# Kernel tuning notes

Hardware: AMD Instinct MI355X
Metric: run time of the kernel (lower is better)

The kernel has to match this reference:

```python
import jax, jax.numpy as jnp
import numpy as np
import math

B, S, CTX, D, H, DH = 2, 2048, 256, 1024, 16, 64
INNER = H * DH
DFF = 4 * D


def layernorm(x, eps=1e-5):
    m = jnp.mean(x, axis=-1, keepdims=True)
    v = jnp.var(x, axis=-1, keepdims=True)
    return (x - m) * jax.lax.rsqrt(v + eps)


def adaln(x, t, w, b):
    # AdaLayerNorm: linear(t) -> (scale, shift); NOTE: original never applies SiLU.
    emb = t @ w + b                       # [B,1,2D]
    scale, shift = jnp.split(emb, 2, axis=-1)
    return layernorm(x) * (1.0 + scale) + shift


def mha(xq, ctx, wq, wk, wv, wo, bo):
    b, sq, _ = xq.shape
    sk = ctx.shape[1]
    q = (xq @ wq).reshape(b, sq, H, DH).transpose(0, 2, 1, 3)   # bhqd
    k = (ctx @ wk).reshape(b, sk, H, DH).transpose(0, 2, 1, 3)  # bhkd
    v = (ctx @ wv).reshape(b, sk, H, DH).transpose(0, 2, 1, 3)
    scores = jnp.einsum('bhqd,bhkd->bhqk', q, k) / math.sqrt(DH)
    attn = jax.nn.softmax(scores, axis=-1)
    out = jnp.einsum('bhqk,bhkd->bhqd', attn, v)
    out = out.transpose(0, 2, 1, 3).reshape(b, sq, INNER)
    return out @ wo + bo


def glu_ff(x, w1, b1, w2, b2):
    u = x @ w1 + b1                       # [B,S,2*DFF]
    a, gate = jnp.split(u, 2, axis=-1)
    return (a * jax.nn.gelu(gate, approximate=False)) @ w2 + b2


def setup_inputs():
    key = jax.random.key(0)
    ks = jax.random.split(key, 24)
    s = 1.0 / math.sqrt(D)

    def n(k, shape, scale=1.0):
        return jax.random.normal(k, shape, dtype=jnp.float32) * scale

    return {
        'x': n(ks[0], (B, S, D)),
        't': n(ks[1], (B, 1, D)),
        'context': n(ks[2], (B, CTX, D)),
        # self-attention (attn1)
        'attn1_wq': n(ks[3], (D, INNER), s),
        'attn1_wk': n(ks[4], (D, INNER), s),
        'attn1_wv': n(ks[5], (D, INNER), s),
        'attn1_wo': n(ks[6], (INNER, D), s),
        'attn1_bo': n(ks[7], (D,), 0.01),
        # cross-attention (attn2)
        'attn2_wq': n(ks[8], (D, INNER), s),
        'attn2_wk': n(ks[9], (D, INNER), s),
        'attn2_wv': n(ks[10], (D, INNER), s),
        'attn2_wo': n(ks[11], (INNER, D), s),
        'attn2_bo': n(ks[12], (D,), 0.01),
        # gated FFN
        'ff_w1': n(ks[13], (D, 2 * DFF), s),
        'ff_b1': n(ks[14], (2 * DFF,), 0.01),
        'ff_w2': n(ks[15], (DFF, D), 1.0 / math.sqrt(DFF)),
        'ff_b2': n(ks[16], (D,), 0.01),
        # AdaLayerNorm linears (D -> 2D)
        'norm1_w': n(ks[17], (D, 2 * D), s),
        'norm1_b': n(ks[18], (2 * D,), 0.01),
        'norm2_w': n(ks[19], (D, 2 * D), s),
        'norm2_b': n(ks[20], (2 * D,), 0.01),
        'norm3_w': n(ks[21], (D, 2 * D), s),
        'norm3_b': n(ks[22], (2 * D,), 0.01),
    }


def reference(x, t, context,
              attn1_wq, attn1_wk, attn1_wv, attn1_wo, attn1_bo,
              attn2_wq, attn2_wk, attn2_wv, attn2_wo, attn2_bo,
              ff_w1, ff_b1, ff_w2, ff_b2,
              norm1_w, norm1_b, norm2_w, norm2_b, norm3_w, norm3_b):
    h1 = adaln(x, t, norm1_w, norm1_b)
    x = mha(h1, h1, attn1_wq, attn1_wk, attn1_wv, attn1_wo, attn1_bo) + x
    h2 = adaln(x, t, norm2_w, norm2_b)
    x = mha(h2, context, attn2_wq, attn2_wk, attn2_wv, attn2_wo, attn2_bo) + x
    h3 = adaln(x, t, norm3_w, norm3_b)
    x = glu_ff(h3, ff_w1, ff_b1, ff_w2, ff_b2) + x
    return x
```

## Files before the change

### kernel.cpp

```cpp
#include <hip/hip_runtime.h>
#include <hip/hip_bf16.h>
#include <math.h>
#include <stdint.h>

typedef __bf16 bf16;
typedef __attribute__((ext_vector_type(8))) __bf16 bf16x8;
typedef __attribute__((ext_vector_type(4))) __bf16 bf16x4;
typedef __attribute__((ext_vector_type(4))) float f32x4;
typedef __attribute__((ext_vector_type(16))) float f32x16;

static constexpr int cB = 2, cS = 2048, cCTX = 256, cD = 1024, cH = 16, cDH = 64, cDFF = 4096;

__device__ __forceinline__ void glds16(const bf16* g, bf16* l) {
  __builtin_amdgcn_global_load_lds(
      (const __attribute__((address_space(1))) void*)g,
      (__attribute__((address_space(3))) void*)l, 16, 0, 0);
}

struct T8 { const float* s[8]; };
__global__ __launch_bounds__(256) void k_transpose8(T8 args, bf16* __restrict__ out) {
  __shared__ bf16 tile[64][66];
  const int n0 = blockIdx.x * 64, k0 = blockIdx.y * 64;
  const int z = blockIdx.z;
  const float* in = args.s[z];
  bf16* dst_base = out + (size_t)z * 1024 * 1024;
  const int t = threadIdx.x;
  const int r = t >> 2, cb = (t & 3) * 16;
  const float* src = in + (size_t)(k0 + r) * 1024 + n0 + cb;
#pragma unroll
  for (int q4 = 0; q4 < 4; ++q4) {
    f32x4 v = *(const f32x4*)(src + q4 * 4);
#pragma unroll
    for (int e = 0; e < 4; ++e) tile[r][cb + q4 * 4 + e] = (bf16)v[e];
  }
  __syncthreads();
  bf16* dst = dst_base + (size_t)(n0 + r) * 1024 + k0 + cb;
  bf16x8 o0, o1;
#pragma unroll
  for (int e = 0; e < 8; ++e) { o0[e] = tile[cb + e][r]; o1[e] = tile[cb + 8 + e][r]; }
  *(bf16x8*)(dst) = o0;
  *(bf16x8*)(dst + 8) = o1;
}

__global__ __launch_bounds__(256) void k_transpose(const float* __restrict__ in,
                                                   bf16* __restrict__ out, int K, int N) {
  __shared__ bf16 tile[64][66];
  const int n0 = blockIdx.x * 64, k0 = blockIdx.y * 64;
  const int t = threadIdx.x;
  const int r = t >> 2, cb = (t & 3) * 16;
  const float* src = in + (size_t)(k0 + r) * N + n0 + cb;
#pragma unroll
  for (int q4 = 0; q4 < 4; ++q4) {
    f32x4 v = *(const f32x4*)(src + q4 * 4);
#pragma unroll
    for (int e = 0; e < 4; ++e) tile[r][cb + q4 * 4 + e] = (bf16)v[e];
  }
  __syncthreads();
  bf16* dst = out + (size_t)(n0 + r) * K + k0 + cb;
  bf16x8 o0, o1;
#pragma unroll
  for (int e = 0; e < 8; ++e) { o0[e] = tile[cb + e][r]; o1[e] = tile[cb + 8 + e][r]; }
  *(bf16x8*)(dst) = o0;
  *(bf16x8*)(dst + 8) = o1;
}

__global__ __launch_bounds__(256) void k_vt(const bf16* __restrict__ V, int vstride,
                                            bf16* __restrict__ VT, int kvlen) {
  __shared__ bf16 tile[64][72];
  const int kt = blockIdx.x * 64, bh = blockIdx.y;
  const int b = bh >> 4, h = bh & 15;
  const int t = threadIdx.x, r = t >> 2, cb = (t & 3) * 16;
  const bf16* src = V + (size_t)(b * kvlen + kt + r) * vstride + h * 64 + cb;
  bf16x8 a0 = *(const bf16x8*)src;
  bf16x8 a1 = *(const bf16x8*)(src + 8);
#pragma unroll
  for (int e = 0; e < 8; ++e) { tile[r][cb + e] = a0[e]; tile[r][cb + 8 + e] = a1[e]; }
  __syncthreads();
  bf16* dst = VT + ((size_t)bh * 64 + r) * kvlen + kt + cb;
  bf16x8 o0, o1;
#pragma unroll
  for (int e = 0; e < 8; ++e) { o0[e] = tile[cb + e][r]; o1[e] = tile[cb + 8 + e][r]; }
  *(bf16x8*)(dst) = o0;
  *(bf16x8*)(dst + 8) = o1;
}

__global__ __launch_bounds__(256) void k_f2b(const float* __restrict__ in, bf16* __restrict__ out) {
  const int base = (blockIdx.x * 256 + threadIdx.x) * 4;
  f32x4 v = *(const f32x4*)(in + base);
  bf16x4 o;
#pragma unroll
  for (int e = 0; e < 4; ++e) o[e] = (bf16)v[e];
  *(bf16x4*)(out + base) = o;
}

struct EmbArgs { const float* w0; const float* w1; const float* w2;
                 const float* b0; const float* b1; const float* b2; };
__global__ __launch_bounds__(256) void k_emb3(const float* __restrict__ t, EmbArgs ea,
                                              float* __restrict__ emb) {
  const int which = blockIdx.y;
  const float* w = which == 0 ? ea.w0 : (which == 1 ? ea.w1 : ea.w2);
  const float* bias = which == 0 ? ea.b0 : (which == 1 ? ea.b1 : ea.b2);
  float* dst = emb + which * 4096;
  const int jj = threadIdx.x & 63;
  const int j = blockIdx.x * 64 + jj;
  const int kg = threadIdx.x >> 6;
  float a0 = 0.f, a1 = 0.f;
  for (int k = kg * 256; k < kg * 256 + 256; ++k) {
    float wv = w[(size_t)k * 2048 + j];
    a0 += t[k] * wv;
    a1 += t[1024 + k] * wv;
  }
  __shared__ float s0[4][64], s1[4][64];
  s0[kg][jj] = a0;
  s1[kg][jj] = a1;
  __syncthreads();
  if (threadIdx.x < 64) {
    dst[j] = s0[0][jj] + s0[1][jj] + s0[2][jj] + s0[3][jj] + bias[j];
    dst[2048 + j] = s1[0][jj] + s1[1][jj] + s1[2][jj] + s1[3][jj] + bias[j];
  }
}

__global__ __launch_bounds__(256) void k_adaln(const float* __restrict__ xres,
                                               const float* __restrict__ emb,
                                               bf16* __restrict__ h) {
  const int token = blockIdx.x;
  const int b = token >> 11;
  const float* x = xres + (size_t)token * 1024;
  const float* sc = emb + b * 2048;
  const int t = threadIdx.x;
  float v[4], s = 0.f, sq = 0.f;
#pragma unroll
  for (int i = 0; i < 4; ++i) {
    float u = x[t + 256 * i];
    v[i] = u; s += u; sq += u * u;
  }
#pragma unroll
  for (int off = 1; off < 64; off <<= 1) {
    s += __shfl_xor(s, off);
    sq += __shfl_xor(sq, off);
  }
  __shared__ float ss[4], ssq[4];
  const int wave = t >> 6;
  if ((t & 63) == 0) { ss[wave] = s; ssq[wave] = sq; }
  __syncthreads();
  const float S_ = ss[0] + ss[1] + ss[2] + ss[3];
  const float SQ = ssq[0] + ssq[1] + ssq[2] + ssq[3];
  const float mean = S_ * (1.f / 1024.f);
  const float var = SQ * (1.f / 1024.f) - mean * mean;
  const float rstd = rsqrtf(var + 1e-5f);
#pragma unroll
  for (int i = 0; i < 4; ++i) {
    const int c = t + 256 * i;
    float val = (v[i] - mean) * rstd * (1.f + sc[c]) + sc[1024 + c];
    h[(size_t)token * 1024 + c] = (bf16)val;
  }
}

template <int TN>
__global__ __launch_bounds__(256) void k_gemm_t(const bf16* __restrict__ A,
                                                const bf16* __restrict__ Bt,
                                                bf16* Cb, float* Cf,
                                                const float* __restrict__ bias,
                                                const float* res,
                                                int M, int N, int K) {
  constexpr int CJ = TN / 64;
  __shared__ bf16 As[2 * 128 * 32];
  __shared__ bf16 Bs[2 * TN * 32];
  const int m0 = blockIdx.y * 128, n0 = blockIdx.x * TN;
  const int tid = threadIdx.x;
  const int wave = tid >> 6, lane = tid & 63;
  const int l31 = lane & 31, hi8 = (lane >> 5) * 8;
  const int mw = (wave >> 1) * 64, nw = (wave & 1) * (TN / 2);
  f32x16 acc[2][CJ];
#pragma unroll
  for (int i = 0; i < 2; ++i)
#pragma unroll
    for (int j = 0; j < CJ; ++j) acc[i][j] = (f32x16)(0.f);

  const int r0 = tid >> 2, c0 = (tid & 3) << 3;
  const bf16* Ap = A + (size_t)(m0 + r0) * K + c0;
  const bf16* Bp = Bt + (size_t)(n0 + r0) * K + c0;
  bf16* lA = As + r0 * 32 + c0;
  bf16* lB = Bs + r0 * 32 + c0;

  for (int k0 = 0; k0 < K; k0 += 64) {
    __syncthreads();
    glds16(Ap + k0, lA);
    glds16(Ap + k0 + (size_t)64 * K, lA + 64 * 32);
    glds16(Ap + k0 + 32, lA + 128 * 32);
    glds16(Ap + k0 + 32 + (size_t)64 * K, lA + 192 * 32);
    glds16(Bp + k0, lB);
    if (TN == 128) glds16(Bp + k0 + (size_t)64 * K, lB + 64 * 32);
    glds16(Bp + k0 + 32, lB + TN * 32);
    if (TN == 128) glds16(Bp + k0 + 32 + (size_t)64 * K, lB + TN * 32 + 64 * 32);
    __syncthreads();
#pragma unroll
    for (int kp = 0; kp < 2; ++kp) {
      const bf16* Asp = As + kp * 128 * 32;
      const bf16* Bsp = Bs + kp * TN * 32;
#pragma unroll
      for (int kh = 0; kh < 2; ++kh) {
        bf16x8 af[2], bfr[CJ];
#pragma unroll
        for (int i = 0; i < 2; ++i)
          af[i] = *(const bf16x8*)(Asp + (mw + i * 32 + l31) * 32 + kh * 16 + hi8);
#pragma unroll
        for (int j = 0; j < CJ; ++j)
          bfr[j] = *(const bf16x8*)(Bsp + (nw + j * 32 + l31) * 32 + kh * 16 + hi8);
#pragma unroll
        for (int i = 0; i < 2; ++i)
#pragma unroll
          for (int j = 0; j < CJ; ++j)
            acc[i][j] = __builtin_amdgcn_mfma_f32_32x32x16_bf16(af[i], bfr[j], acc[i][j], 0, 0, 0);
      }
    }
  }

#pragma unroll
  for (int i = 0; i < 2; ++i) {
    const int rb = m0 + mw + i * 32 + 4 * (lane >> 5);
#pragma unroll
    for (int j = 0; j < CJ; ++j) {
      const int col = n0 + nw + j * 32 + l31;
      const float bv = bias ? bias[col] : 0.f;
#pragma unroll
      for (int reg = 0; reg < 16; ++reg) {
        const int row = rb + (reg & 3) + 8 * (reg >> 2);
        const size_t off = (size_t)row * N + col;
        float v2 = acc[i][j][reg] + bv;
        if (res) v2 += res[off];
        if (Cf) Cf[off] = v2;
        if (Cb) Cb[off] = (bf16)v2;
      }
    }
  }
}

__global__ __launch_bounds__(512, 2) void k_glu8(const bf16* __restrict__ A,
                                                 const bf16* __restrict__ Bt,
                                                 const float* __restrict__ bias,
                                                 bf16* __restrict__ C) {
  constexpr int K = 1024, NOUT = 4096, NT = K / 64, NIT = NT / 2;
  __shared__ __align__(16) bf16 sA[2 * 2 * 8192];
  __shared__ __align__(16) bf16 sB[2 * 2 * 8192];

  const int bid = blockIdx.x;
  const int xcd = bid & 7, bj = bid >> 3;
  const int n_idx = xcd * 4 + (bj >> 4);
  const int m_idx = bj & 15;
  const int m0 = m_idx * 256, n0 = n_idx * 128;

  const int tid = threadIdx.x;
  const int wid = tid >> 6, lane = tid & 63;
  const int l15 = lane & 15, hi = lane >> 4;
  const int wm = wid >> 2, wn = wid & 3;

  const int srA = wid * 32 + (lane >> 2);
  const int scol = (lane & 3) * 8;
  const bf16* aS0 = A + (size_t)(m0 + srA) * K + scol;
  const bf16* aS1 = aS0 + (size_t)16 * K;
  auto grow = [&](int r) {
    return n0 + (r >> 6) * 32 + (r & 31) + ((r & 32) ? NOUT : 0);
  };
  const bf16* bS0 = Bt + (size_t)grow(srA) * K + scol;
  const bf16* bS1 = Bt + (size_t)grow(srA + 16) * K + scol;
  bf16* aD = sA + wid * 1024 + lane * 8;
  bf16* bD = sB + wid * 1024 + lane * 8;
  const bf16* aF = sA + (wm * 128 + l15) * 32 + hi * 8;
  const bf16* bF = sB + (wn * 64 + l15) * 32 + hi * 8;

  f32x4 acc[8][4];
#pragma unroll
  for (int i = 0; i < 8; ++i)
#pragma unroll
    for (int n = 0; n < 4; ++n) acc[i][n] = (f32x4){0.f, 0.f, 0.f, 0.f};
  bf16x8 aq[4], bq[4];

#define STG_A(bb, kh, kt) do { \
    glds16(aS0 + (kt) * 64 + (kh) * 32, aD + ((bb) * 2 + (kh)) * 8192); \
    glds16(aS1 + (kt) * 64 + (kh) * 32, aD + ((bb) * 2 + (kh)) * 8192 + 512); } while (0)
#define STG_B(bb, kh, kt) do { \
    glds16(bS0 + (kt) * 64 + (kh) * 32, bD + ((bb) * 2 + (kh)) * 8192); \
    glds16(bS1 + (kt) * 64 + (kh) * 32, bD + ((bb) * 2 + (kh)) * 8192 + 512); } while (0)

#define PH(bb, kh, mh, STAGES, VMC) do { \
    if ((mh) == 0) { \
      _Pragma("unroll") \
      for (int nf = 0; nf < 4; ++nf) \
        bq[nf] = *(const bf16x8*)(bF + ((bb) * 2 + (kh)) * 8192 + nf * 512); \
    } \
    _Pragma("unroll") \
    for (int mi = 0; mi < 4; ++mi) \
      aq[mi] = *(const bf16x8*)(aF + ((bb) * 2 + (kh)) * 8192 + ((mh) * 4 + mi) * 512); \
    STAGES; \
    __builtin_amdgcn_s_barrier(); \
    asm volatile("s_waitcnt lgkmcnt(0)" ::: "memory"); \
    __builtin_amdgcn_sched_barrier(0); \
    __builtin_amdgcn_s_setprio(1); \
    _Pragma("unroll") \
    for (int mi = 0; mi < 4; ++mi) \
      _Pragma("unroll") \
      for (int nf = 0; nf < 4; ++nf) \
        acc[(mh) * 4 + mi][nf] = __builtin_amdgcn_mfma_f32_16x16x32_bf16( \
            aq[mi], bq[nf], acc[(mh) * 4 + mi][nf], 0, 0, 0); \
    __builtin_amdgcn_s_setprio(0); \
    VMC; \
    __builtin_amdgcn_s_barrier(); \
    __builtin_amdgcn_sched_barrier(0); \
  } while (0)

  STG_B(0, 0, 0); STG_A(0, 0, 0); STG_B(0, 1, 0); STG_A(0, 1, 0);
  STG_B(1, 0, 1); STG_A(1, 0, 1); STG_B(1, 1, 1);
  asm volatile("s_waitcnt vmcnt(6)" ::: "memory");
  __builtin_amdgcn_s_barrier();
  __builtin_amdgcn_sched_barrier(0);

  for (int it = 0; it < NIT; ++it) {
    const int T = 2 * it;
    const int t2 = (T + 2 < NT) ? (T + 2) : 0;
    const int t3 = (T + 3 < NT) ? (T + 3) : 0;
    PH(0, 0, 0, STG_A(1, 1, T + 1), );
    PH(0, 0, 1, STG_B(0, 0, t2), );
    PH(0, 1, 0, STG_A(0, 0, t2), );
    PH(0, 1, 1, STG_B(0, 1, t2), asm volatile("s_waitcnt vmcnt(6)" ::: "memory"));
    PH(1, 0, 0, STG_A(0, 1, t2), );
    PH(1, 0, 1, STG_B(1, 0, t3), );
    PH(1, 1, 0, STG_A(1, 0, t3), );
    PH(1, 1, 1, STG_B(1, 1, t3), asm volatile("s_waitcnt vmcnt(6)" ::: "memory"));
  }
#undef PH
#undef STG_A
#undef STG_B

#pragma unroll
  for (int mi = 0; mi < 8; ++mi) {
    const int row = m0 + wm * 128 + mi * 16 + hi * 4;
#pragma unroll
    for (int nf = 0; nf < 2; ++nf) {
      const int col = n0 + wn * 32 + nf * 16 + l15;
      const float bav = bias[col], bgv = bias[NOUT + col];
#pragma unroll
      for (int r = 0; r < 4; ++r) {
        float a = acc[mi][nf][r] + bav;
        float g = acc[mi][nf + 2][r] + bgv;
        float ge = 0.5f * g * (1.0f + erff(g * 0.70710678118654752f));
        C[(size_t)(row + r) * NOUT + col] = (bf16)(a * ge);
      }
    }
  }
}

__global__ __launch_bounds__(256) void k_attn(const bf16* __restrict__ Qp, int qstride,
                                              const bf16* __restrict__ Kp, int kstride,
                                              const bf16* __restrict__ VTp,
                                              bf16* __restrict__ Op, int kvlen) {
  const int qt = blockIdx.x * 128;
  const int hd = blockIdx.y;
  const int b = blockIdx.z;
  const int tid = threadIdx.x;
  const int wave = tid >> 6, lane = tid & 63;
  const int quad = lane >> 4, l16 = lane & 15;

  __shared__ __align__(16) bf16 Ks[64 * 64];
  __shared__ __align__(16) bf16 Vs[64 * 64];
  __shared__ __align__(16) bf16 Ps[4][32 * 72];

  bf16x8 qf[2][2];
#pragma unroll
  for (int g = 0; g < 2; ++g) {
    const bf16* qrow = Qp + (size_t)(b * cS + qt + wave * 32 + g * 16 + l16) * qstride + hd * 64;
#pragma unroll
    for (int c = 0; c < 2; ++c) {
      bf16x8 raw = *(const bf16x8*)(qrow + c * 32 + quad * 8);
#pragma unroll
      for (int e = 0; e < 8; ++e) qf[g][c][e] = (bf16)((float)raw[e] * 0.125f);
    }
  }

  float l_part[2][4] = {{0.f, 0.f, 0.f, 0.f}, {0.f, 0.f, 0.f, 0.f}};
  f32x4 o_acc[2][4];
#pragma unroll
  for (int g = 0; g < 2; ++g)
#pragma unroll
    for (int n = 0; n < 4; ++n) o_acc[g][n] = (f32x4){0.f, 0.f, 0.f, 0.f};

  const int lrow = wave * 16 + (lane >> 3);
  const int lcol = (lane & 7) * 8;
  const bf16* kbase = Kp + (size_t)(b * kvlen + lrow) * kstride + hd * 64 + lcol;
  const bf16* vbase = VTp + ((size_t)((b * 16 + hd) * 64 + lrow)) * kvlen + lcol;
  bf16* lk = Ks + lrow * 64 + lcol;
  bf16* lv = Vs + lrow * 64 + lcol;

  for (int kt = 0; kt < kvlen; kt += 64) {
    __syncthreads();
    const bf16* kg = kbase + (size_t)kt * kstride;
    glds16(kg, lk);
    glds16(kg + (size_t)8 * kstride, lk + 8 * 64);
    glds16(vbase + kt, lv);
    glds16(vbase + kt + (size_t)8 * kvlen, lv + 8 * 64);
    __syncthreads();

    f32x4 s[2][4];
#pragma unroll
    for (int g = 0; g < 2; ++g)
#pragma unroll
      for (int t = 0; t < 4; ++t) s[g][t] = (f32x4){0.f, 0.f, 0.f, 0.f};
#pragma unroll
    for (int t = 0; t < 4; ++t)
#pragma unroll
      for (int c = 0; c < 2; ++c) {
        bf16x8 kf = *(const bf16x8*)(Ks + (t * 16 + l16) * 64 + c * 32 + quad * 8);
#pragma unroll
        for (int g = 0; g < 2; ++g)
          s[g][t] = __builtin_amdgcn_mfma_f32_16x16x32_bf16(qf[g][c], kf, s[g][t], 0, 0, 0);
      }

#pragma unroll
    for (int g = 0; g < 2; ++g)
#pragma unroll
      for (int t = 0; t < 4; ++t)
#pragma unroll
        for (int r = 0; r < 4; ++r) {
          float p = __expf(s[g][t][r]);
          Ps[wave][(g * 16 + quad * 4 + r) * 72 + t * 16 + l16] = (bf16)p;
          l_part[g][r] += p;
        }

    bf16x8 pf[2][2];
#pragma unroll
    for (int g = 0; g < 2; ++g)
#pragma unroll
      for (int c = 0; c < 2; ++c)
        pf[g][c] = *(const bf16x8*)(&Ps[wave][(g * 16 + l16) * 72 + c * 32 + quad * 8]);
#pragma unroll
    for (int n = 0; n < 4; ++n)
#pragma unroll
      for (int c = 0; c < 2; ++c) {
        bf16x8 vf = *(const bf16x8*)(Vs + (n * 16 + l16) * 64 + c * 32 + quad * 8);
#pragma unroll
        for (int g = 0; g < 2; ++g)
          o_acc[g][n] = __builtin_amdgcn_mfma_f32_16x16x32_bf16(pf[g][c], vf, o_acc[g][n], 0, 0, 0);
      }
  }

#pragma unroll
  for (int g = 0; g < 2; ++g) {
    float rl[4];
#pragma unroll
    for (int r = 0; r < 4; ++r) {
      float v = l_part[g][r];
      v += __shfl_xor(v, 1);
      v += __shfl_xor(v, 2);
      v += __shfl_xor(v, 4);
      v += __shfl_xor(v, 8);
      rl[r] = 1.f / v;
    }
#pragma unroll
    for (int n = 0; n < 4; ++n)
#pragma unroll
      for (int r = 0; r < 4; ++r) {
        const int srow = qt + wave * 32 + g * 16 + quad * 4 + r;
        const int d = n * 16 + l16;
        Op[(size_t)(b * cS + srow) * 1024 + hd * 64 + d] = (bf16)(o_acc[g][n][r] * rl[r]);
      }
  }
}

extern "C" void kernel_launch(void* const* d_in, const int* in_sizes, int n_in,
                              void* d_out, int out_size, void* d_ws, size_t ws_size,
                              hipStream_t stream) {
  const float* x    = (const float*)d_in[0];
  const float* tt   = (const float*)d_in[1];
  const float* ctx  = (const float*)d_in[2];
  const float* fw1  = (const float*)d_in[13];
  const float* fb1  = (const float*)d_in[14];
  const float* fw2  = (const float*)d_in[15];
  const float* fb2  = (const float*)d_in[16];
  const float* a1bo = (const float*)d_in[7];
  const float* a2bo = (const float*)d_in[12];

  char* ws = (char*)d_ws;
  const size_t MB = 1ull << 20;
  bf16* wsq   = (bf16*)(ws + 0 * MB);
  bf16* wqkv1 = wsq;
  bf16* wto1  = (bf16*)(ws + 6 * MB);
  bf16* wtq2  = (bf16*)(ws + 8 * MB);
  bf16* wkv2w = (bf16*)(ws + 10 * MB);
  bf16* wto2  = (bf16*)(ws + 14 * MB);
  bf16* wtf1  = (bf16*)(ws + 16 * MB);
  bf16* wtf2  = (bf16*)(ws + 32 * MB);
  float* emb  = (float*)(ws + 40 * MB);
  float* emb1 = emb, *emb2 = emb + 4096, *emb3 = emb + 8192;
  bf16* ctxb  = (bf16*)(ws + 40 * MB + 262144);
  float* xres = (float*)(ws + 42 * MB);
  bf16* h     = (bf16*)(ws + 58 * MB);
  bf16* ao    = h;
  bf16* qkv   = (bf16*)(ws + 66 * MB);
  bf16* q2    = qkv;
  bf16* vT1   = (bf16*)(ws + 90 * MB);
  bf16* kv2   = (bf16*)(ws + 0 * MB);
  bf16* vT2   = (bf16*)(ws + 2 * MB);
  bf16* g     = (bf16*)(ws + 66 * MB);
  float* out  = (float*)d_out;

  const dim3 blk(256);

  T8 t8;
  t8.s[0] = (const float*)d_in[3];
  t8.s[1] = (const float*)d_in[4];
  t8.s[2] = (const float*)d_in[5];
  t8.s[3] = (const float*)d_in[6];
  t8.s[4] = (const float*)d_in[8];
  t8.s[5] = (const float*)d_in[9];
  t8.s[6] = (const float*)d_in[10];
  t8.s[7] = (const float*)d_in[11];
  k_transpose8<<<dim3(16, 16, 8), blk, 0, stream>>>(t8, wsq);
  k_transpose<<<dim3(128, 16), blk, 0, stream>>>(fw1, wtf1, 1024, 8192);
  k_transpose<<<dim3(16, 64), blk, 0, stream>>>(fw2, wtf2, 4096, 1024);

  EmbArgs ea;
  ea.w0 = (const float*)d_in[17]; ea.b0 = (const float*)d_in[18];
  ea.w1 = (const float*)d_in[19]; ea.b1 = (const float*)d_in[20];
  ea.w2 = (const float*)d_in[21]; ea.b2 = (const float*)d_in[22];
  k_emb3<<<dim3(32, 3), blk, 0, stream>>>(tt, ea, emb);
  k_f2b<<<512, blk, 0, stream>>>(ctx, ctxb);

  k_adaln<<<4096, blk, 0, stream>>>(x, emb1, h);
  k_gemm_t<128><<<dim3(24, 32), blk, 0, stream>>>(h, wqkv1, qkv, nullptr, nullptr, nullptr, 4096, 3072, 1024);
  k_vt<<<dim3(32, 32), blk, 0, stream>>>(qkv + 2048, 3072, vT1, 2048);
  k_attn<<<dim3(16, 16, 2), blk, 0, stream>>>(qkv, 3072, qkv + 1024, 3072, vT1, ao, 2048);
  k_gemm_t<64><<<dim3(16, 32), blk, 0, stream>>>(ao, wto1, nullptr, xres, a1bo, x, 4096, 1024, 1024);

  k_adaln<<<4096, blk, 0, stream>>>(xres, emb2, h);
  k_gemm_t<64><<<dim3(16, 32), blk, 0, stream>>>(h, wtq2, q2, nullptr, nullptr, nullptr, 4096, 1024, 1024);
  k_gemm_t<128><<<dim3(16, 4), blk, 0, stream>>>(ctxb, wkv2w, kv2, nullptr, nullptr, nullptr, 512, 2048, 1024);
  k_vt<<<dim3(4, 32), blk, 0, stream>>>(kv2 + 1024, 2048, vT2, 256);
  k_attn<<<dim3(16, 16, 2), blk, 0, stream>>>(q2, 1024, kv2, 2048, vT2, ao, 256);
  k_gemm_t<64><<<dim3(16, 32), blk, 0, stream>>>(ao, wto2, nullptr, xres, a2bo, xres, 4096, 1024, 1024);

  k_adaln<<<4096, blk, 0, stream>>>(xres, emb3, h);
  k_glu8<<<dim3(512), dim3(512), 0, stream>>>(h, wtf1, fb1, g);
  k_gemm_t<64><<<dim3(16, 32), blk, 0, stream>>>(g, wtf2, nullptr, out, fb2, xres, 4096, 1024, 4096);
}
```

Baseline: 639.4 us.

## Double-buffer LDS in GEMM and attention, add XOR swizzles against bank conflicts

Adds an optional double-buffered LDS pipeline to the generic GEMM: the next K tile is prefetched while the current one is computed, and it is enabled for the TN=64 launches. The attention kernel gets double-buffered K/V tiles plus an XOR column swizzle on staging and fragment reads. The GLU kernel also gets an XOR swizzle on its global-load-to-LDS addresses. The goal is to overlap global loads with MFMA work and cut LDS bank conflicts, at the cost of more LDS per block and possibly lower occupancy.

```diff
diff --git a/kernel.cpp b/kernel.cpp
--- a/kernel.cpp
+++ b/kernel.cpp
@@ -156,7 +156,7 @@
   }
 }
 
-template <int TN>
+template <int TN, int DB>
 __global__ __launch_bounds__(256) void k_gemm_t(const bf16* __restrict__ A,
                                                 const bf16* __restrict__ Bt,
                                                 bf16* Cb, float* Cf,
@@ -164,8 +164,8 @@
                                                 const float* res,
                                                 int M, int N, int K) {
   constexpr int CJ = TN / 64;
-  __shared__ bf16 As[2 * 128 * 32];
-  __shared__ bf16 Bs[2 * TN * 32];
+  __shared__ bf16 As[DB][2 * 128 * 32];
+  __shared__ bf16 Bs[DB][2 * TN * 32];
   const int m0 = blockIdx.y * 128, n0 = blockIdx.x * TN;
   const int tid = threadIdx.x;
   const int wave = tid >> 6, lane = tid & 63;
@@ -180,41 +180,66 @@
   const int r0 = tid >> 2, c0 = (tid & 3) << 3;
   const bf16* Ap = A + (size_t)(m0 + r0) * K + c0;
   const bf16* Bp = Bt + (size_t)(n0 + r0) * K + c0;
-  bf16* lA = As + r0 * 32 + c0;
-  bf16* lB = Bs + r0 * 32 + c0;
-
-  for (int k0 = 0; k0 < K; k0 += 64) {
+  bf16* lA0 = &As[0][0] + r0 * 32 + c0;
+  bf16* lB0 = &Bs[0][0] + r0 * 32 + c0;
+
+#define STAGE_GT(buf, k0)                                                       \
+  do {                                                                          \
+    bf16* lA = lA0 + (buf) * (2 * 128 * 32);                                    \
+    bf16* lB = lB0 + (buf) * (2 * TN * 32);                                     \
+    glds16(Ap + (k0), lA);                                                      \
+    glds16(Ap + (k0) + (size_t)64 * K, lA + 64 * 32);                           \
+    glds16(Ap + (k0) + 32, lA + 128 * 32);                                      \
+    glds16(Ap + (k0) + 32 + (size_t)64 * K, lA + 192 * 32);                     \
+    glds16(Bp + (k0), lB);                                                      \
+    if (TN == 128) glds16(Bp + (k0) + (size_t)64 * K, lB + 64 * 32);            \
+    glds16(Bp + (k0) + 32, lB + TN * 32);                                       \
+    if (TN == 128) glds16(Bp + (k0) + 32 + (size_t)64 * K, lB + TN * 32 + 64 * 32); \
+  } while (0)
+
+#define COMPUTE_GT(buf)                                                          \
+  do {                                                                           \
+    _Pragma("unroll")                                                            \
+    for (int kp = 0; kp < 2; ++kp) {                                             \
+      const bf16* Asp = &As[buf][0] + kp * 128 * 32;                             \
+      const bf16* Bsp = &Bs[buf][0] + kp * TN * 32;                              \
+      _Pragma("unroll")                                                          \
+      for (int kh = 0; kh < 2; ++kh) {                                           \
+        bf16x8 af[2], bfr[CJ];                                                   \
+        _Pragma("unroll")                                                        \
+        for (int i = 0; i < 2; ++i)                                              \
+          af[i] = *(const bf16x8*)(Asp + (mw + i * 32 + l31) * 32 + kh * 16 + hi8); \
+        _Pragma("unroll")                                                        \
+        for (int j = 0; j < CJ; ++j)                                             \
+          bfr[j] = *(const bf16x8*)(Bsp + (nw + j * 32 + l31) * 32 + kh * 16 + hi8); \
+        _Pragma("unroll")                                                        \
+        for (int i = 0; i < 2; ++i)                                              \
+          _Pragma("unroll")                                                      \
+          for (int j = 0; j < CJ; ++j)                                           \
+            acc[i][j] = __builtin_amdgcn_mfma_f32_32x32x16_bf16(af[i], bfr[j], acc[i][j], 0, 0, 0); \
+      }                                                                          \
+    }                                                                            \
+  } while (0)
+
+  if (DB == 2) {
+    STAGE_GT(0, 0);
     __syncthreads();
-    glds16(Ap + k0, lA);
-    glds16(Ap + k0 + (size_t)64 * K, lA + 64 * 32);
-    glds16(Ap + k0 + 32, lA + 128 * 32);
-    glds16(Ap + k0 + 32 + (size_t)64 * K, lA + 192 * 32);
-    glds16(Bp + k0, lB);
-    if (TN == 128) glds16(Bp + k0 + (size_t)64 * K, lB + 64 * 32);
-    glds16(Bp + k0 + 32, lB + TN * 32);
-    if (TN == 128) glds16(Bp + k0 + 32 + (size_t)64 * K, lB + TN * 32 + 64 * 32);
-    __syncthreads();
-#pragma unroll
-    for (int kp = 0; kp < 2; ++kp) {
-      const bf16* Asp = As + kp * 128 * 32;
-      const bf16* Bsp = Bs + kp * TN * 32;
-#pragma unroll
-      for (int kh = 0; kh < 2; ++kh) {
-        bf16x8 af[2], bfr[CJ];
-#pragma unroll
-        for (int i = 0; i < 2; ++i)
-          af[i] = *(const bf16x8*)(Asp + (mw + i * 32 + l31) * 32 + kh * 16 + hi8);
-#pragma unroll
-        for (int j = 0; j < CJ; ++j)
-          bfr[j] = *(const bf16x8*)(Bsp + (nw + j * 32 + l31) * 32 + kh * 16 + hi8);
-#pragma unroll
-        for (int i = 0; i < 2; ++i)
-#pragma unroll
-          for (int j = 0; j < CJ; ++j)
-            acc[i][j] = __builtin_amdgcn_mfma_f32_32x32x16_bf16(af[i], bfr[j], acc[i][j], 0, 0, 0);
-      }
+    for (int k0 = 0; k0 < K; k0 += 64) {
+      const int cur = (k0 >> 6) & 1;
+      if (k0 + 64 < K) STAGE_GT(cur ^ 1, k0 + 64);
+      COMPUTE_GT(cur);
+      __syncthreads();
     }
-  }
+  } else {
+    for (int k0 = 0; k0 < K; k0 += 64) {
+      __syncthreads();
+      STAGE_GT(0, k0);
+      __syncthreads();
+      COMPUTE_GT(0);
+    }
+  }
+#undef STAGE_GT
+#undef COMPUTE_GT
 
 #pragma unroll
   for (int i = 0; i < 2; ++i) {
@@ -256,7 +281,7 @@
   const int wm = wid >> 2, wn = wid & 3;
 
   const int srA = wid * 32 + (lane >> 2);
-  const int scol = (lane & 3) * 8;
+  const int scol = ((lane & 3) ^ ((lane >> 3) & 3)) * 8;
   const bf16* aS0 = A + (size_t)(m0 + srA) * K + scol;
   const bf16* aS1 = aS0 + (size_t)16 * K;
   auto grow = [&](int r) {
@@ -266,8 +291,9 @@
   const bf16* bS1 = Bt + (size_t)grow(srA + 16) * K + scol;
   bf16* aD = sA + wid * 1024 + lane * 8;
   bf16* bD = sB + wid * 1024 + lane * 8;
-  const bf16* aF = sA + (wm * 128 + l15) * 32 + hi * 8;
-  const bf16* bF = sB + (wn * 64 + l15) * 32 + hi * 8;
+  const int rxor = (hi ^ ((l15 >> 1) & 3)) * 8;
+  const bf16* aF = sA + (wm * 128 + l15) * 32 + rxor;
+  const bf16* bF = sB + (wn * 64 + l15) * 32 + rxor;
 
   f32x4 acc[8][4];
 #pragma unroll
@@ -360,9 +386,10 @@
   const int tid = threadIdx.x;
   const int wave = tid >> 6, lane = tid & 63;
   const int quad = lane >> 4, l16 = lane & 15;
-
-  __shared__ __align__(16) bf16 Ks[64 * 64];
-  __shared__ __align__(16) bf16 Vs[64 * 64];
+  const int rswq = l16 & 7;
+
+  __shared__ __align__(16) bf16 Ks[2][64 * 64];
+  __shared__ __align__(16) bf16 Vs[2][64 * 64];
   __shared__ __align__(16) bf16 Ps[4][32 * 72];
 
   bf16x8 qf[2][2];
@@ -386,19 +413,29 @@
 
   const int lrow = wave * 16 + (lane >> 3);
   const int lcol = (lane & 7) * 8;
-  const bf16* kbase = Kp + (size_t)(b * kvlen + lrow) * kstride + hd * 64 + lcol;
-  const bf16* vbase = VTp + ((size_t)((b * 16 + hd) * 64 + lrow)) * kvlen + lcol;
-  bf16* lk = Ks + lrow * 64 + lcol;
-  bf16* lv = Vs + lrow * 64 + lcol;
+  const int scol = (((lane & 7) ^ ((lane >> 3) & 7)) * 8);
+  const bf16* kbase = Kp + (size_t)(b * kvlen + lrow) * kstride + hd * 64 + scol;
+  const bf16* vbase = VTp + ((size_t)((b * 16 + hd) * 64 + lrow)) * kvlen + scol;
+  bf16* lk0 = &Ks[0][0] + lrow * 64 + lcol;
+  bf16* lv0 = &Vs[0][0] + lrow * 64 + lcol;
+
+#define STAGE_AT(buf, kt)                                              \
+  do {                                                                 \
+    const bf16* kg = kbase + (size_t)(kt) * kstride;                   \
+    bf16* lk = lk0 + (buf) * (64 * 64);                                \
+    bf16* lv = lv0 + (buf) * (64 * 64);                                \
+    glds16(kg, lk);                                                    \
+    glds16(kg + (size_t)8 * kstride, lk + 8 * 64);                     \
+    glds16(vbase + (kt), lv);                                          \
+    glds16(vbase + (kt) + (size_t)8 * kvlen, lv + 8 * 64);             \
+  } while (0)
+
+  STAGE_AT(0, 0);
+  __syncthreads();
 
   for (int kt = 0; kt < kvlen; kt += 64) {
-    __syncthreads();
-    const bf16* kg = kbase + (size_t)kt * kstride;
-    glds16(kg, lk);
-    glds16(kg + (size_t)8 * kstride, lk + 8 * 64);
-    glds16(vbase + kt, lv);
-    glds16(vbase + kt + (size_t)8 * kvlen, lv + 8 * 64);
-    __syncthreads();
+    const int cur = (kt >> 6) & 1;
+    if (kt + 64 < kvlen) STAGE_AT(cur ^ 1, kt + 64);
 
     f32x4 s[2][4];
 #pragma unroll
@@ -409,7 +446,7 @@
     for (int t = 0; t < 4; ++t)
 #pragma unroll
       for (int c = 0; c < 2; ++c) {
-        bf16x8 kf = *(const bf16x8*)(Ks + (t * 16 + l16) * 64 + c * 32 + quad * 8);
+        bf16x8 kf = *(const bf16x8*)(&Ks[cur][0] + (t * 16 + l16) * 64 + (((c * 4 + quad) ^ rswq) << 3));
 #pragma unroll
         for (int g = 0; g < 2; ++g)
           s[g][t] = __builtin_amdgcn_mfma_f32_16x16x32_bf16(qf[g][c], kf, s[g][t], 0, 0, 0);
@@ -436,12 +473,14 @@
     for (int n = 0; n < 4; ++n)
 #pragma unroll
       for (int c = 0; c < 2; ++c) {
-        bf16x8 vf = *(const bf16x8*)(Vs + (n * 16 + l16) * 64 + c * 32 + quad * 8);
+        bf16x8 vf = *(const bf16x8*)(&Vs[cur][0] + (n * 16 + l16) * 64 + (((c * 4 + quad) ^ rswq) << 3));
 #pragma unroll
         for (int g = 0; g < 2; ++g)
           o_acc[g][n] = __builtin_amdgcn_mfma_f32_16x16x32_bf16(pf[g][c], vf, o_acc[g][n], 0, 0, 0);
       }
-  }
+    __syncthreads();
+  }
+#undef STAGE_AT
 
 #pragma unroll
   for (int g = 0; g < 2; ++g) {
@@ -526,19 +565,19 @@
   k_f2b<<<512, blk, 0, stream>>>(ctx, ctxb);
 
   k_adaln<<<4096, blk, 0, stream>>>(x, emb1, h);
-  k_gemm_t<128><<<dim3(24, 32), blk, 0, stream>>>(h, wqkv1, qkv, nullptr, nullptr, nullptr, 4096, 3072, 1024);
+  k_gemm_t<128, 1><<<dim3(24, 32), blk, 0, stream>>>(h, wqkv1, qkv, nullptr, nullptr, nullptr, 4096, 3072, 1024);
   k_vt<<<dim3(32, 32), blk, 0, stream>>>(qkv + 2048, 3072, vT1, 2048);
   k_attn<<<dim3(16, 16, 2), blk, 0, stream>>>(qkv, 3072, qkv + 1024, 3072, vT1, ao, 2048);
-  k_gemm_t<64><<<dim3(16, 32), blk, 0, stream>>>(ao, wto1, nullptr, xres, a1bo, x, 4096, 1024, 1024);
+  k_gemm_t<64, 2><<<dim3(16, 32), blk, 0, stream>>>(ao, wto1, nullptr, xres, a1bo, x, 4096, 1024, 1024);
 
   k_adaln<<<4096, blk, 0, stream>>>(xres, emb2, h);
-  k_gemm_t<64><<<dim3(16, 32), blk, 0, stream>>>(h, wtq2, q2, nullptr, nullptr, nullptr, 4096, 1024, 1024);
-  k_gemm_t<128><<<dim3(16, 4), blk, 0, stream>>>(ctxb, wkv2w, kv2, nullptr, nullptr, nullptr, 512, 2048, 1024);
+  k_gemm_t<64, 2><<<dim3(16, 32), blk, 0, stream>>>(h, wtq2, q2, nullptr, nullptr, nullptr, 4096, 1024, 1024);
+  k_gemm_t<128, 1><<<dim3(16, 4), blk, 0, stream>>>(ctxb, wkv2w, kv2, nullptr, nullptr, nullptr, 512, 2048, 1024);
   k_vt<<<dim3(4, 32), blk, 0, stream>>>(kv2 + 1024, 2048, vT2, 256);
   k_attn<<<dim3(16, 16, 2), blk, 0, stream>>>(q2, 1024, kv2, 2048, vT2, ao, 256);
-  k_gemm_t<64><<<dim3(16, 32), blk, 0, stream>>>(ao, wto2, nullptr, xres, a2bo, xres, 4096, 1024, 1024);
+  k_gemm_t<64, 2><<<dim3(16, 32), blk, 0, stream>>>(ao, wto2, nullptr, xres, a2bo, xres, 4096, 1024, 1024);
 
   k_adaln<<<4096, blk, 0, stream>>>(xres, emb3, h);
   k_glu8<<<dim3(512), dim3(512), 0, stream>>>(h, wtf1, fb1, g);
-  k_gemm_t<64><<<dim3(16, 32), blk, 0, stream>>>(g, wtf2, nullptr, out, fb2, xres, 4096, 1024, 4096);
-}
+  k_gemm_t<64, 2><<<dim3(16, 32), blk, 0, stream>>>(g, wtf2, nullptr, out, fb2, xres, 4096, 1024, 4096);
+}
```

Result: faster. 611.6 us (-4.3%).
